# Performance work log

Hardware: AMD Instinct MI355X
Metric: run time of the kernel (lower is better)

Reference implementation:

```python
import math
import jax, jax.numpy as jnp
import numpy as np

B, N, L, E, H, T = 64, 8, 128, 768, 12, 64


def setup_inputs() -> dict:
    key = jax.random.key(0)
    ks = jax.random.split(key, 8)
    s = 0.02
    return {
        "x":  jax.random.normal(ks[0], (B, N, L, E), dtype=jnp.float32),
        # torch Linear weights are [out, in]
        "Wq": jax.random.normal(ks[1], (H, E, E), dtype=jnp.float32) * s,
        "bq": jax.random.normal(ks[2], (H, E), dtype=jnp.float32) * s,
        "Wv": jax.random.normal(ks[3], (H, T, E), dtype=jnp.float32) * s,
        "bv": jax.random.normal(ks[4], (H, T), dtype=jnp.float32) * s,
        "Wf": jax.random.normal(ks[5], (E, H * T), dtype=jnp.float32) * s,
        "bf": jax.random.normal(ks[6], (E,), dtype=jnp.float32) * s,
    }


def reference(x, Wq, bq, Wv, bv, Wf, bf):
    b, n, l, e = x.shape
    S = b * n                      # set_size after the view(-1, L, E)
    x2 = x.reshape(S, l, e)
    # per-head query projection (batched over heads)
    Q = jnp.einsum('sle,hfe->hslf', x2, Wq) + bq[:, None, None, :]      # [H,S,L,E]
    # raw (unsoftmaxed) attention: (Q K^T) V / sqrt(E)
    scores = jnp.einsum('hslf,smf->hslm', Q, x2)                        # [H,S,L,L]
    attn = jnp.einsum('hslm,sme->hsle', scores, x2) * (1.0 / math.sqrt(e))
    # per-head value projection to transformer_dim
    V = jnp.einsum('hsle,hte->hslt', attn, Wv) + bv[:, None, None, :]   # [H,S,L,T]
    # concat heads along last dim (head order preserved)
    cat = jnp.transpose(V, (1, 2, 0, 3)).reshape(S, l, -1)              # [S,L,H*T]
    out = cat @ Wf.T + bf                                               # [S,L,E]
    return out.reshape(b, n, l, e)
```

## Files before the change

### kernel.cpp

```cpp
#include <hip/hip_runtime.h>
#include <stdint.h>


#define EE 768
#define SLOT 50331648L

typedef short s16x8 __attribute__((ext_vector_type(8)));
typedef float f32x4 __attribute__((ext_vector_type(4)));

__device__ __forceinline__ short f2bf(float f){
  union { float fv; uint32_t u; } v; v.fv = f;
  uint32_t r = (v.u + 0x7fffu + ((v.u >> 16) & 1u)) >> 16;
  return (short)r;
}

__device__ __forceinline__ void gld_lds16(const short* g, short* l){
  __builtin_amdgcn_global_load_lds(
      (const __attribute__((address_space(1))) void*)(uintptr_t)g,
      (__attribute__((address_space(3))) void*)(uintptr_t)l,
      16, 0, 0);
}

__device__ __forceinline__ int xcd_swz(int bid, int nwg){
  int xcd = bid & 7, loc = bid >> 3;
  int q = nwg >> 3, r = nwg & 7;
  return (xcd < r ? xcd * (q + 1) : r * (q + 1) + (xcd - r) * q) + loc;
}

__device__ __forceinline__ int swz64(int row, int c){ return c ^ ((row & 7) << 3); }
__device__ __forceinline__ int swz32(int row, int c){ return c ^ (((row >> 1) & 3) << 3); }

__global__ __launch_bounds__(256) void cast_bf16_k(const float* __restrict__ src,
                                                   short* __restrict__ dst,
                                                   long n, float scale){
  long i = ((long)blockIdx.x * 256 + threadIdx.x) * 8;
  if(i >= n) return;
  float4 a = *(const float4*)(src + i);
  float4 b = *(const float4*)(src + i + 4);
  s16x8 o;
  o[0]=f2bf(a.x*scale); o[1]=f2bf(a.y*scale); o[2]=f2bf(a.z*scale); o[3]=f2bf(a.w*scale);
  o[4]=f2bf(b.x*scale); o[5]=f2bf(b.y*scale); o[6]=f2bf(b.z*scale); o[7]=f2bf(b.w*scale);
  *(s16x8*)(dst + i) = o;
}

__global__ __launch_bounds__(256) void cvec_k(const float* __restrict__ Wf,
                                              const float* __restrict__ bv,
                                              const float* __restrict__ bfv,
                                              float* __restrict__ c){
  int e = blockIdx.x * 256 + threadIdx.x;
  if(e >= EE) return;
  float s = bfv[e];
  for(int k = 0; k < EE; ++k) s += Wf[(long)e * EE + k] * bv[k];
  c[e] = s;
}

__global__ __launch_bounds__(256) void bias_build(const float* __restrict__ bq,
                                                  float* __restrict__ biasQP){
  int i = blockIdx.x * 256 + threadIdx.x;
  if(i < 9984) biasQP[i] = (i < 9216) ? bq[i] : 0.f;
}

__global__ __launch_bounds__(512, 1) void gemm8p(const short* __restrict__ A,
                                                 const short* __restrict__ W,
                                                 const float* __restrict__ bias,
                                                 short* __restrict__ OutBase,
                                                 int hBase, int nSub, int pSub){
  extern __shared__ short lds[];
  const int tid = threadIdx.x, lane = tid & 63, w = tid >> 6;
  const int wr = w >> 2, wc = w & 3;
  const int bid = xcd_swz(blockIdx.x, nSub * 768);
  const int g = bid / 768, rb = bid - g * 768;
  const int rowBlk = rb / 3, colBlk = rb - rowBlk * 3;
  const long rowA0 = (long)rowBlk * 256;
  const int colB0 = colBlk * 256;
  const int wh = (g == pSub) ? 12 : hBase + g;
  const short* Bm = W + (long)wh * 589824L;

  const int srow = tid >> 3;
  const int ssw = swz64(srow, (tid & 7) * 8);
  const short* gA = A + (rowA0 + srow) * 768 + ssw;
  const short* gB = Bm + (long)(colB0 + srow) * 768 + ssw;

  auto stageH = [&](int b, int kt, int which){
    const short* gs = (which < 2 ? gA : gB) + (long)(which & 1) * 98304 + kt;
    short* dst = lds + b * 32768 + (which >> 1) * 16384 + (which & 1) * 8192 + w * 512;
    gld_lds16(gs, dst);
    gld_lds16(gs + 49152, dst + 4096);
  };

  f32x4 acc[8][4] = {};
  const int fr = lane & 15, fcb = (lane >> 4) * 8;
  s16x8 af[4][2], bf[2][2];

  auto readA = [&](int b, int mh){
    const short* Al = lds + b * 32768;
    #pragma unroll
    for(int m = 0; m < 4; ++m){
      int row = wr * 128 + (mh * 4 + m) * 16 + fr;
      #pragma unroll
      for(int kk = 0; kk < 2; ++kk)
        af[m][kk] = *(const s16x8*)&Al[row * 64 + swz64(row, kk * 32 + fcb)];
    }
  };
  auto readB = [&](int b, int nh){
    const short* Bl = lds + b * 32768 + 16384;
    #pragma unroll
    for(int n = 0; n < 2; ++n){
      int row = wc * 64 + (nh * 2 + n) * 16 + fr;
      #pragma unroll
      for(int kk = 0; kk < 2; ++kk)
        bf[n][kk] = *(const s16x8*)&Bl[row * 64 + swz64(row, kk * 32 + fcb)];
    }
  };
  auto mmq = [&](int mh, int nh){
    asm volatile("s_waitcnt lgkmcnt(0)" ::: "memory");
    __builtin_amdgcn_s_setprio(1);
    #pragma unroll
    for(int m = 0; m < 4; ++m)
      #pragma unroll
      for(int n = 0; n < 2; ++n)
        #pragma unroll
        for(int kk = 0; kk < 2; ++kk)
          acc[mh*4+m][nh*2+n] = __builtin_amdgcn_mfma_f32_16x16x32_bf16(
              af[m][kk], bf[n][kk], acc[mh*4+m][nh*2+n], 0, 0, 0);
    __builtin_amdgcn_s_setprio(0);
  };

  stageH(0, 0, 0); stageH(0, 0, 1); stageH(0, 0, 2); stageH(0, 0, 3);

  for(int t = 0; t < 12; ++t){
    const int b = t & 1, nb = b ^ 1;
    const int kt1 = (t + 1) * 64;
    if(t < 11){
      stageH(nb, kt1, 0);
      asm volatile("s_waitcnt vmcnt(2)" ::: "memory");
    } else {
      asm volatile("s_waitcnt vmcnt(0)" ::: "memory");
    }
    asm volatile("s_barrier" ::: "memory");
    readA(b, 0); readB(b, 0);
    mmq(0, 0);
    asm volatile("s_barrier" ::: "memory");
    readB(b, 1);
    if(t < 11) stageH(nb, kt1, 1);
    asm volatile("s_barrier" ::: "memory");
    mmq(0, 1);
    asm volatile("s_barrier" ::: "memory");
    readA(b, 1);
    if(t < 11) stageH(nb, kt1, 2);
    asm volatile("s_barrier" ::: "memory");
    mmq(1, 1);
    asm volatile("s_barrier" ::: "memory");
    readB(b, 0);
    if(t < 11) stageH(nb, kt1, 3);
    asm volatile("s_barrier" ::: "memory");
    mmq(1, 0);
    asm volatile("s_barrier" ::: "memory");
  }

  asm volatile("s_waitcnt vmcnt(0) lgkmcnt(0)" ::: "memory");
  __syncthreads();

  float bb[4];
  #pragma unroll
  for(int n = 0; n < 4; ++n)
    bb[n] = bias[wh * 768 + colB0 + wc * 64 + n * 16 + fr];

  short* Out = OutBase + (long)g * SLOT;
  short* Cs = lds;
  #pragma unroll
  for(int ch = 0; ch < 2; ++ch){
    __syncthreads();
    if(wr == ch){
      #pragma unroll
      for(int m = 0; m < 8; ++m)
        #pragma unroll
        for(int n = 0; n < 4; ++n)
          #pragma unroll
          for(int r2 = 0; r2 < 4; ++r2){
            int row = m * 16 + (lane >> 4) * 4 + r2;
            int c = wc * 64 + n * 16 + fr;
            Cs[row * 256 + (c ^ (((row >> 2) & 3) << 4))] = f2bf(acc[m][n][r2] + bb[n]);
          }
    }
    __syncthreads();
    #pragma unroll
    for(int i = 0; i < 8; ++i){
      int idx = i * 512 + tid;
      int row = idx >> 5, cl = (idx & 31) * 8;
      s16x8 v = *(const s16x8*)&Cs[row * 256 + (cl ^ (((row >> 2) & 3) << 4))];
      *(s16x8*)&Out[(rowA0 + ch * 128 + row) * 768 + colB0 + cl] = v;
    }
  }
}

__global__ __launch_bounds__(512, 1) void gemm256(const short* __restrict__ A,
                                                  const short* __restrict__ W,
                                                  const float* __restrict__ bias,
                                                  short* __restrict__ OutBase,
                                                  int hBase, int nSub, int pSub){
  __shared__ short lds[2][16384];
  const int tid = threadIdx.x, lane = tid & 63, w = tid >> 6;
  const int wr = w >> 2, wc = w & 3;
  const int bid = xcd_swz(blockIdx.x, nSub * 768);
  const int g = bid / 768, rb = bid - g * 768;
  const int rowBlk = rb / 3, colBlk = rb - rowBlk * 3;
  const long rowA0 = (long)rowBlk * 256;
  const int colB0 = colBlk * 256;
  const int wh = (g == pSub) ? 12 : hBase + g;
  const short* Bm = W + (long)wh * 589824L;
  short* Out = OutBase + (long)g * SLOT;

  const int sr0 = w * 32 + (lane >> 2);
  const int sr1 = sr0 + 16;
  const int scol = (lane & 3) * 8;
  const int sc0 = swz32(sr0, scol);
  const int sc1 = swz32(sr1, scol);
  const short* Ar0 = A + (rowA0 + sr0) * 768;
  const short* Ar1 = A + (rowA0 + sr1) * 768;
  const short* Br0 = Bm + (long)(colB0 + sr0) * 768;
  const short* Br1 = Bm + (long)(colB0 + sr1) * 768;

  f32x4 acc[8][4] = {};
  s16x8 af[4], bf0[2], bf1[2];
  const int fr = lane & 15, fc = (lane >> 4) * 8;

  auto stage = [&](int b, int kt){
    short* Al = &lds[b][0];
    short* Bl = &lds[b][8192];
    gld_lds16(Ar0 + kt + sc0, Al + (w * 2) * 512);
    gld_lds16(Ar1 + kt + sc1, Al + (w * 2 + 1) * 512);
    gld_lds16(Br0 + kt + sc0, Bl + (w * 2) * 512);
    gld_lds16(Br1 + kt + sc1, Bl + (w * 2 + 1) * 512);
  };

  stage(0, 0);
  for(int t = 0; t < 24; ++t){
    if(t < 23){
      stage((t + 1) & 1, (t + 1) * 32);
      asm volatile("s_waitcnt vmcnt(4)\n\ts_barrier" ::: "memory");
    } else {
      asm volatile("s_waitcnt vmcnt(0)\n\ts_barrier" ::: "memory");
    }
    const short* Al = &lds[t & 1][0];
    const short* Bl = &lds[t & 1][8192];

    auto loadA = [&](int mh){
      #pragma unroll
      for(int m = 0; m < 4; ++m){
        int row = wr * 128 + (mh * 4 + m) * 16 + fr;
        af[m] = *(const s16x8*)&Al[row * 32 + swz32(row, fc)];
      }
    };
    auto loadB = [&](int nh, s16x8* bf){
      #pragma unroll
      for(int n = 0; n < 2; ++n){
        int row = wc * 64 + (nh * 2 + n) * 16 + fr;
        bf[n] = *(const s16x8*)&Bl[row * 32 + swz32(row, fc)];
      }
    };
    auto mm = [&](int mh, int nh, s16x8* bf){
      __builtin_amdgcn_s_setprio(1);
      #pragma unroll
      for(int m = 0; m < 4; ++m)
        #pragma unroll
        for(int n = 0; n < 2; ++n)
          acc[mh * 4 + m][nh * 2 + n] = __builtin_amdgcn_mfma_f32_16x16x32_bf16(
              af[m], bf[n], acc[mh * 4 + m][nh * 2 + n], 0, 0, 0);
      __builtin_amdgcn_s_setprio(0);
    };

    loadA(0); loadB(0, bf0); mm(0, 0, bf0);
    loadB(1, bf1);           mm(0, 1, bf1);
    loadA(1);                mm(1, 1, bf1);
    loadB(0, bf0);           mm(1, 0, bf0);
    asm volatile("s_barrier" ::: "memory");
  }

  float bb[4];
  #pragma unroll
  for(int n = 0; n < 4; ++n)
    bb[n] = bias[wh * 768 + colB0 + wc * 64 + n * 16 + fr];

  short* Cs = &lds[0][0];
  #pragma unroll
  for(int ch = 0; ch < 2; ++ch){
    __syncthreads();
    if(wr == ch){
      #pragma unroll
      for(int m = 0; m < 8; ++m)
        #pragma unroll
        for(int n = 0; n < 4; ++n)
          #pragma unroll
          for(int r2 = 0; r2 < 4; ++r2){
            int row = m * 16 + (lane >> 4) * 4 + r2;
            int c = wc * 64 + n * 16 + fr;
            Cs[row * 256 + (c ^ (((row >> 2) & 3) << 4))] = f2bf(acc[m][n][r2] + bb[n]);
          }
    }
    __syncthreads();
    #pragma unroll
    for(int i = 0; i < 8; ++i){
      int idx = i * 512 + tid;
      int row = idx >> 5, cl = (idx & 31) * 8;
      s16x8 v = *(const s16x8*)&Cs[row * 256 + (cl ^ (((row >> 2) & 3) << 4))];
      *(s16x8*)&Out[(rowA0 + ch * 128 + row) * 768 + colB0 + cl] = v;
    }
  }
}

__global__ __launch_bounds__(256, 2) void gemm_f32(const short* __restrict__ A,
                                                   const short* __restrict__ B,
                                                   const float* __restrict__ bias,
                                                   float* __restrict__ Cout){
  __shared__ short smem[4 * 8192];
  const int tid = threadIdx.x, lane = tid & 63, w = tid >> 6;
  const int wr = w >> 1, wc = w & 1;
  const int nCol = 6;
  const int xcd = blockIdx.x & 7, loc = blockIdx.x >> 3;
  const int width = nCol << 3;
  const int gid = loc / width, rem = loc % width;
  const int rowBlk = (xcd << 6) + (gid << 3) + (rem & 7);
  const int colBlk = rem >> 3;
  const long rowA0 = (long)rowBlk << 7;
  const long colB0 = (long)colBlk << 7;
  const int lr = lane >> 3;
  const int sA = swz64(lr, (lane & 7) * 8);

  f32x4 acc[4][4] = {};
  auto stage = [&](int b, int kt){
    short* As = smem + b * 16384;
    #pragma unroll
    for(int it = 0; it < 4; ++it){
      int r = it * 32 + w * 8;
      gld_lds16(&A[(rowA0 + r + lr) * 768 + kt + sA], &As[r * 64]);
      gld_lds16(&B[(colB0 + r + lr) * 768 + kt + sA], &As[8192 + r * 64]);
    }
  };

  stage(0, 0);
  for(int t = 0; t < 12; ++t){
    const int cur = t & 1;
    if(t < 11){
      stage(cur ^ 1, (t + 1) * 64);
      asm volatile("s_waitcnt vmcnt(8)\n\ts_barrier" ::: "memory");
    } else {
      asm volatile("s_waitcnt vmcnt(0)\n\ts_barrier" ::: "memory");
    }
    const short* As = smem + cur * 16384;
    const short* Bs = As + 8192;
    #pragma unroll
    for(int kk = 0; kk < 2; ++kk){
      s16x8 af[4], bfr[4];
      #pragma unroll
      for(int m = 0; m < 4; ++m){
        int row = wr * 64 + m * 16 + (lane & 15);
        af[m] = *(const s16x8*)&As[row * 64 + swz64(row, kk * 32 + (lane >> 4) * 8)];
      }
      #pragma unroll
      for(int n = 0; n < 4; ++n){
        int row = wc * 64 + n * 16 + (lane & 15);
        bfr[n] = *(const s16x8*)&Bs[row * 64 + swz64(row, kk * 32 + (lane >> 4) * 8)];
      }
      #pragma unroll
      for(int m = 0; m < 4; ++m)
        #pragma unroll
        for(int n = 0; n < 4; ++n)
          acc[m][n] = __builtin_amdgcn_mfma_f32_16x16x32_bf16(af[m], bfr[n], acc[m][n], 0, 0, 0);
    }
    asm volatile("s_barrier" ::: "memory");
  }

  const long crow0 = rowA0 + wr * 64;
  const long ccol0 = colB0 + wc * 64;
  #pragma unroll
  for(int n = 0; n < 4; ++n){
    const long col = ccol0 + n * 16 + (lane & 15);
    const float bbv = bias[col];
    #pragma unroll
    for(int m = 0; m < 4; ++m)
      #pragma unroll
      for(int r = 0; r < 4; ++r){
        const long row = crow0 + m * 16 + (lane >> 4) * 4 + r;
        Cout[row * 768 + col] = acc[m][n][r] + bbv;
      }
  }
}

__global__ __launch_bounds__(256, 2) void attn_k(const short* __restrict__ Q,
                                                 const short* __restrict__ P,
                                                 const short* __restrict__ X,
                                                 short* __restrict__ Cat,
                                                 int h0, int nH){
  __shared__ short smem[4 * 8192];
  const int tid = threadIdx.x, lane = tid & 63, w = tid >> 6;
  const int wr = w >> 1, wc = w & 1;
  const int nwg = nH << 9;
  const int bid = xcd_swz(blockIdx.x, nwg);
  const int s = bid / nH, hi = bid - s * nH, h = h0 + hi;
  const long row0 = (long)s * 128;
  const int lr = lane >> 3;
  const int sA = swz64(lr, (lane & 7) * 8);

  const int pm = tid >> 3, pt0 = (tid & 7) * 8;
  s16x8 pv[4];
  #pragma unroll
  for(int i = 0; i < 4; ++i)
    pv[i] = *(const s16x8*)&P[(row0 + pm + i * 32) * 768L + h * 64 + pt0];

  f32x4 acc[4][4] = {};
  const short* Qh = Q + (long)hi * SLOT;
  auto stage = [&](int b, int kt){
    short* As = smem + b * 16384;
    #pragma unroll
    for(int it = 0; it < 4; ++it){
      int r = it * 32 + w * 8;
      gld_lds16(&Qh[(row0 + r + lr) * 768L + kt + sA], &As[r * 64]);
      gld_lds16(&X[(row0 + r + lr) * 768L + kt + sA], &As[8192 + r * 64]);
    }
  };

  stage(0, 0);
  for(int t = 0; t < 12; ++t){
    const int cur = t & 1;
    if(t < 11){
      stage(cur ^ 1, (t + 1) * 64);
      asm volatile("s_waitcnt vmcnt(8)\n\ts_barrier" ::: "memory");
    } else {
      asm volatile("s_waitcnt vmcnt(0)\n\ts_barrier" ::: "memory");
    }
    const short* As = smem + cur * 16384;
    const short* Bs = As + 8192;
    #pragma unroll
    for(int kk = 0; kk < 2; ++kk){
      s16x8 af[4], bfr[4];
      #pragma unroll
      for(int m = 0; m < 4; ++m){
        int row = wr * 64 + m * 16 + (lane & 15);
        af[m] = *(const s16x8*)&As[row * 64 + swz64(row, kk * 32 + (lane >> 4) * 8)];
      }
      #pragma unroll
      for(int n = 0; n < 4; ++n){
        int row = wc * 64 + n * 16 + (lane & 15);
        bfr[n] = *(const s16x8*)&Bs[row * 64 + swz64(row, kk * 32 + (lane >> 4) * 8)];
      }
      #pragma unroll
      for(int m = 0; m < 4; ++m)
        #pragma unroll
        for(int n = 0; n < 4; ++n)
          acc[m][n] = __builtin_amdgcn_mfma_f32_16x16x32_bf16(af[m], bfr[n], acc[m][n], 0, 0, 0);
    }
    asm volatile("s_barrier" ::: "memory");
  }

  short* Pt = smem;
  short* Vt = smem + 8192;
  short* Ss = smem + 16384;

  #pragma unroll
  for(int m = 0; m < 4; ++m)
    #pragma unroll
    for(int n = 0; n < 4; ++n)
      #pragma unroll
      for(int r = 0; r < 4; ++r){
        int row = wr * 64 + m * 16 + (lane >> 4) * 4 + r;
        int c = wc * 64 + n * 16 + (lane & 15);
        Ss[row * 128 + swz64(row, c)] = f2bf(acc[m][n][r]);
      }
  #pragma unroll
  for(int i = 0; i < 4; ++i)
    #pragma unroll
    for(int j = 0; j < 8; ++j){
      int trow = pt0 + j;
      int mc = pm + i * 32;
      Pt[trow * 128 + swz64(trow, mc)] = pv[i][j];
    }
  __syncthreads();

  f32x4 accv[2][4] = {};
  #pragma unroll
  for(int kk = 0; kk < 4; ++kk){
    s16x8 a2[2], b4[4];
    #pragma unroll
    for(int m = 0; m < 2; ++m){
      int row = w * 32 + m * 16 + (lane & 15);
      a2[m] = *(const s16x8*)&Ss[row * 128 + swz64(row, kk * 32 + (lane >> 4) * 8)];
    }
    #pragma unroll
    for(int n = 0; n < 4; ++n){
      int trow = n * 16 + (lane & 15);
      b4[n] = *(const s16x8*)&Pt[trow * 128 + swz64(trow, kk * 32 + (lane >> 4) * 8)];
    }
    #pragma unroll
    for(int m = 0; m < 2; ++m)
      #pragma unroll
      for(int n = 0; n < 4; ++n)
        accv[m][n] = __builtin_amdgcn_mfma_f32_16x16x32_bf16(a2[m], b4[n], accv[m][n], 0, 0, 0);
  }

  #pragma unroll
  for(int m = 0; m < 2; ++m)
    #pragma unroll
    for(int n = 0; n < 4; ++n)
      #pragma unroll
      for(int r = 0; r < 4; ++r){
        int row = w * 32 + m * 16 + (lane >> 4) * 4 + r;
        int c = n * 16 + (lane & 15);
        Vt[row * 64 + swz64(row, c)] = f2bf(accv[m][n][r]);
      }
  __syncthreads();
  #pragma unroll
  for(int k2 = 0; k2 < 4; ++k2){
    int row = k2 * 32 + (tid >> 3);
    int cl = (tid & 7) * 8;
    s16x8 v = *(const s16x8*)&Vt[row * 64 + swz64(row, cl)];
    *(s16x8*)&Cat[(row0 + row) * 768L + h * 64 + cl] = v;
  }
}

extern "C" void kernel_launch(void* const* d_in, const int* in_sizes, int n_in,
                              void* d_out, int out_size, void* d_ws, size_t ws_size,
                              hipStream_t stream){
  const float* x  = (const float*)d_in[0];
  const float* Wq = (const float*)d_in[1];
  const float* bq = (const float*)d_in[2];
  const float* Wv = (const float*)d_in[3];
  const float* bv = (const float*)d_in[4];
  const float* Wf = (const float*)d_in[5];
  const float* bfv= (const float*)d_in[6];

  const float rsqE = 0.03608439182435161f;
  char* ws = (char*)d_ws;

  short* Xb  = (short*)(ws);
  short* Cat = (short*)(ws + 100663296L);
  short* Wb  = (short*)(ws + 201326592L);
  short* Wfb = (short*)(ws + 216662016L);
  float* bQP = (float*)(ws + 217841664L);
  float* cv  = (float*)(ws + 217881600L);
  short* QS  = (short*)(ws + 217884672L);

  const size_t QOFF = 217884672ULL;
  int G = 1;
  const int cands[5] = {12, 6, 4, 3, 2};
  for(int i = 0; i < 5; ++i)
    if(ws_size >= QOFF + (size_t)(cands[i] + 1) * 100663296ULL){ G = cands[i]; break; }
  short* Pall = QS + (long)G * SLOT;

  bool deep = hipFuncSetAttribute(reinterpret_cast<const void*>(&gemm8p),
                  hipFuncAttributeMaxDynamicSharedMemorySize, 131072) == hipSuccess;

  dim3 b256(256), b512(512);
  cast_bf16_k<<<24576, b256, 0, stream>>>(x,  Xb, 50331648L, 1.f);
  cast_bf16_k<<<3456,  b256, 0, stream>>>(Wq, Wb, 7077888L, 1.f);
  cast_bf16_k<<<288,   b256, 0, stream>>>(Wv, Wb + 7077888L, 589824L, rsqE);
  cast_bf16_k<<<288,   b256, 0, stream>>>(Wf, Wfb, 589824L, 1.f);
  bias_build<<<39, b256, 0, stream>>>(bq, bQP);
  cvec_k<<<3, b256, 0, stream>>>(Wf, bv, bfv, cv);

  const int nB = 12 / G;
  for(int b = 0; b < nB; ++b){
    const int nSub = G + (b == 0 ? 1 : 0);
    const int pSub = (b == 0) ? G : -1;
    if(deep)
      gemm8p<<<dim3(nSub * 768), b512, 131072, stream>>>(Xb, Wb, bQP, QS, b * G, nSub, pSub);
    else
      gemm256<<<dim3(nSub * 768), b512, 0, stream>>>(Xb, Wb, bQP, QS, b * G, nSub, pSub);
    attn_k<<<dim3(G * 512), b256, 0, stream>>>(QS, Pall, Xb, Cat, b * G, G);
  }
  gemm_f32<<<dim3(3072), b256, 0, stream>>>(Cat, Wfb, cv, (float*)d_out);
}
```

Baseline: 1.680 ms.

## Pipeline attention QK stage in quarters and reuse deep GEMM for final projection

The attention kernel's first GEMM loop now issues its next-tile loads in four chunks spread across four MFMA quarter-steps. Each quarter reads only half of the A and B fragments and raises wave priority during MFMA, so loads overlap compute instead of waiting on one bulk prefetch. The final output projection now runs through the templated deep-LDS gemm8p kernel, which writes fp32 directly, in place of the separate gemm_f32 kernel. The cost is more barriers per k-step, and the fp32 epilogue stores straight from registers without LDS staging, which may reduce store coalescing.

New measurement: 1.671 ms. About the same (-0.5%).

```diff
diff --git a/kernel.cpp b/kernel.cpp
--- a/kernel.cpp
+++ b/kernel.cpp
@@ -60,10 +60,11 @@
   if(i < 9984) biasQP[i] = (i < 9216) ? bq[i] : 0.f;
 }
 
+template<bool OUTF32>
 __global__ __launch_bounds__(512, 1) void gemm8p(const short* __restrict__ A,
                                                  const short* __restrict__ W,
                                                  const float* __restrict__ bias,
-                                                 short* __restrict__ OutBase,
+                                                 void* __restrict__ OutBase,
                                                  int hBase, int nSub, int pSub){
   extern __shared__ short lds[];
   const int tid = threadIdx.x, lane = tid & 63, w = tid >> 6;
@@ -166,31 +167,45 @@
   for(int n = 0; n < 4; ++n)
     bb[n] = bias[wh * 768 + colB0 + wc * 64 + n * 16 + fr];
 
-  short* Out = OutBase + (long)g * SLOT;
-  short* Cs = lds;
-  #pragma unroll
-  for(int ch = 0; ch < 2; ++ch){
-    __syncthreads();
-    if(wr == ch){
-      #pragma unroll
-      for(int m = 0; m < 8; ++m)
+  if constexpr(!OUTF32){
+    short* Out = (short*)OutBase + (long)g * SLOT;
+    short* Cs = lds;
+    #pragma unroll
+    for(int ch = 0; ch < 2; ++ch){
+      __syncthreads();
+      if(wr == ch){
         #pragma unroll
-        for(int n = 0; n < 4; ++n)
+        for(int m = 0; m < 8; ++m)
           #pragma unroll
-          for(int r2 = 0; r2 < 4; ++r2){
-            int row = m * 16 + (lane >> 4) * 4 + r2;
-            int c = wc * 64 + n * 16 + fr;
-            Cs[row * 256 + (c ^ (((row >> 2) & 3) << 4))] = f2bf(acc[m][n][r2] + bb[n]);
-          }
-    }
-    __syncthreads();
-    #pragma unroll
-    for(int i = 0; i < 8; ++i){
-      int idx = i * 512 + tid;
-      int row = idx >> 5, cl = (idx & 31) * 8;
-      s16x8 v = *(const s16x8*)&Cs[row * 256 + (cl ^ (((row >> 2) & 3) << 4))];
-      *(s16x8*)&Out[(rowA0 + ch * 128 + row) * 768 + colB0 + cl] = v;
-    }
+          for(int n = 0; n < 4; ++n)
+            #pragma unroll
+            for(int r2 = 0; r2 < 4; ++r2){
+              int row = m * 16 + (lane >> 4) * 4 + r2;
+              int c = wc * 64 + n * 16 + fr;
+              Cs[row * 256 + (c ^ (((row >> 2) & 3) << 4))] = f2bf(acc[m][n][r2] + bb[n]);
+            }
+      }
+      __syncthreads();
+      #pragma unroll
+      for(int i = 0; i < 8; ++i){
+        int idx = i * 512 + tid;
+        int row = idx >> 5, cl = (idx & 31) * 8;
+        s16x8 v = *(const s16x8*)&Cs[row * 256 + (cl ^ (((row >> 2) & 3) << 4))];
+        *(s16x8*)&Out[(rowA0 + ch * 128 + row) * 768 + colB0 + cl] = v;
+      }
+    }
+  } else {
+    float* Co = (float*)OutBase;
+    #pragma unroll
+    for(int m = 0; m < 8; ++m)
+      #pragma unroll
+      for(int n = 0; n < 4; ++n)
+        #pragma unroll
+        for(int r2 = 0; r2 < 4; ++r2){
+          const long row = rowA0 + wr * 128 + m * 16 + (lane >> 4) * 4 + r2;
+          const int col = colB0 + wc * 64 + n * 16 + fr;
+          Co[row * 768 + col] = acc[m][n][r2] + bb[n];
+        }
   }
 }
 
@@ -399,8 +414,6 @@
   const int bid = xcd_swz(blockIdx.x, nwg);
   const int s = bid / nH, hi = bid - s * nH, h = h0 + hi;
   const long row0 = (long)s * 128;
-  const int lr = lane >> 3;
-  const int sA = swz64(lr, (lane & 7) * 8);
 
   const int pm = tid >> 3, pt0 = (tid & 7) * 8;
   s16x8 pv[4];
@@ -408,50 +421,90 @@
   for(int i = 0; i < 4; ++i)
     pv[i] = *(const s16x8*)&P[(row0 + pm + i * 32) * 768L + h * 64 + pt0];
 
+  const short* Qh = Q + (long)hi * SLOT;
+  const int srow = tid >> 3;
+  const int ssw = swz64(srow, (tid & 7) * 8);
+  const short* gQ = Qh + (row0 + srow) * 768 + ssw;
+  const short* gX = X + (row0 + srow) * 768 + ssw;
+
+  auto stageQX = [&](int b, int kt, int j){
+    short* As = smem + b * 16384;
+    gld_lds16(gQ + (long)j * 24576 + kt, As + j * 2048 + w * 512);
+    gld_lds16(gX + (long)j * 24576 + kt, As + 8192 + j * 2048 + w * 512);
+  };
+
   f32x4 acc[4][4] = {};
-  const short* Qh = Q + (long)hi * SLOT;
-  auto stage = [&](int b, int kt){
-    short* As = smem + b * 16384;
-    #pragma unroll
-    for(int it = 0; it < 4; ++it){
-      int r = it * 32 + w * 8;
-      gld_lds16(&Qh[(row0 + r + lr) * 768L + kt + sA], &As[r * 64]);
-      gld_lds16(&X[(row0 + r + lr) * 768L + kt + sA], &As[8192 + r * 64]);
-    }
-  };
-
-  stage(0, 0);
+  const int fr = lane & 15, fcb = (lane >> 4) * 8;
+  s16x8 af[2][2], bf[2][2];
+
+  auto readAq = [&](int b, int mh){
+    const short* Al = smem + b * 16384;
+    #pragma unroll
+    for(int m = 0; m < 2; ++m){
+      int row = wr * 64 + (mh * 2 + m) * 16 + fr;
+      #pragma unroll
+      for(int kk = 0; kk < 2; ++kk)
+        af[m][kk] = *(const s16x8*)&Al[row * 64 + swz64(row, kk * 32 + fcb)];
+    }
+  };
+  auto readBq = [&](int b, int nh){
+    const short* Bl = smem + b * 16384 + 8192;
+    #pragma unroll
+    for(int n = 0; n < 2; ++n){
+      int row = wc * 64 + (nh * 2 + n) * 16 + fr;
+      #pragma unroll
+      for(int kk = 0; kk < 2; ++kk)
+        bf[n][kk] = *(const s16x8*)&Bl[row * 64 + swz64(row, kk * 32 + fcb)];
+    }
+  };
+  auto mmq = [&](int mh, int nh){
+    asm volatile("s_waitcnt lgkmcnt(0)" ::: "memory");
+    __builtin_amdgcn_s_setprio(1);
+    #pragma unroll
+    for(int m = 0; m < 2; ++m)
+      #pragma unroll
+      for(int n = 0; n < 2; ++n)
+        #pragma unroll
+        for(int kk = 0; kk < 2; ++kk)
+          acc[mh*2+m][nh*2+n] = __builtin_amdgcn_mfma_f32_16x16x32_bf16(
+              af[m][kk], bf[n][kk], acc[mh*2+m][nh*2+n], 0, 0, 0);
+    __builtin_amdgcn_s_setprio(0);
+  };
+
+  stageQX(0, 0, 0); stageQX(0, 0, 1); stageQX(0, 0, 2); stageQX(0, 0, 3);
+
   for(int t = 0; t < 12; ++t){
-    const int cur = t & 1;
+    const int b = t & 1, nb = b ^ 1;
+    const int kt1 = (t + 1) * 64;
     if(t < 11){
-      stage(cur ^ 1, (t + 1) * 64);
-      asm volatile("s_waitcnt vmcnt(8)\n\ts_barrier" ::: "memory");
+      stageQX(nb, kt1, 0);
+      asm volatile("s_waitcnt vmcnt(2)" ::: "memory");
     } else {
-      asm volatile("s_waitcnt vmcnt(0)\n\ts_barrier" ::: "memory");
-    }
-    const short* As = smem + cur * 16384;
-    const short* Bs = As + 8192;
-    #pragma unroll
-    for(int kk = 0; kk < 2; ++kk){
-      s16x8 af[4], bfr[4];
-      #pragma unroll
-      for(int m = 0; m < 4; ++m){
-        int row = wr * 64 + m * 16 + (lane & 15);
-        af[m] = *(const s16x8*)&As[row * 64 + swz64(row, kk * 32 + (lane >> 4) * 8)];
-      }
-      #pragma unroll
-      for(int n = 0; n < 4; ++n){
-        int row = wc * 64 + n * 16 + (lane & 15);
-        bfr[n] = *(const s16x8*)&Bs[row * 64 + swz64(row, kk * 32 + (lane >> 4) * 8)];
-      }
-      #pragma unroll
-      for(int m = 0; m < 4; ++m)
-        #pragma unroll
-        for(int n = 0; n < 4; ++n)
-          acc[m][n] = __builtin_amdgcn_mfma_f32_16x16x32_bf16(af[m], bfr[n], acc[m][n], 0, 0, 0);
-    }
-    asm volatile("s_barrier" ::: "memory");
-  }
+      asm volatile("s_waitcnt vmcnt(0)" ::: "memory");
+    }
+    asm volatile("s_barrier" ::: "memory");
+    readAq(b, 0); readBq(b, 0);
+    mmq(0, 0);
+    asm volatile("s_barrier" ::: "memory");
+    readBq(b, 1);
+    if(t < 11) stageQX(nb, kt1, 1);
+    asm volatile("s_barrier" ::: "memory");
+    mmq(0, 1);
+    asm volatile("s_barrier" ::: "memory");
+    readAq(b, 1);
+    if(t < 11) stageQX(nb, kt1, 2);
+    asm volatile("s_barrier" ::: "memory");
+    mmq(1, 1);
+    asm volatile("s_barrier" ::: "memory");
+    readBq(b, 0);
+    if(t < 11) stageQX(nb, kt1, 3);
+    asm volatile("s_barrier" ::: "memory");
+    mmq(1, 0);
+    asm volatile("s_barrier" ::: "memory");
+  }
+
+  asm volatile("s_waitcnt vmcnt(0) lgkmcnt(0)" ::: "memory");
+  __syncthreads();
 
   short* Pt = smem;
   short* Vt = smem + 8192;
@@ -547,8 +600,11 @@
     if(ws_size >= QOFF + (size_t)(cands[i] + 1) * 100663296ULL){ G = cands[i]; break; }
   short* Pall = QS + (long)G * SLOT;
 
-  bool deep = hipFuncSetAttribute(reinterpret_cast<const void*>(&gemm8p),
-                  hipFuncAttributeMaxDynamicSharedMemorySize, 131072) == hipSuccess;
+  bool deep =
+      hipFuncSetAttribute(reinterpret_cast<const void*>(&gemm8p<false>),
+                          hipFuncAttributeMaxDynamicSharedMemorySize, 131072) == hipSuccess &&
+      hipFuncSetAttribute(reinterpret_cast<const void*>(&gemm8p<true>),
+                          hipFuncAttributeMaxDynamicSharedMemorySize, 131072) == hipSuccess;
 
   dim3 b256(256), b512(512);
   cast_bf16_k<<<24576, b256, 0, stream>>>(x,  Xb, 50331648L, 1.f);
@@ -563,10 +619,13 @@
     const int nSub = G + (b == 0 ? 1 : 0);
     const int pSub = (b == 0) ? G : -1;
     if(deep)
-      gemm8p<<<dim3(nSub * 768), b512, 131072, stream>>>(Xb, Wb, bQP, QS, b * G, nSub, pSub);
+      gemm8p<false><<<dim3(nSub * 768), b512, 131072, stream>>>(Xb, Wb, bQP, QS, b * G, nSub, pSub);
     else
       gemm256<<<dim3(nSub * 768), b512, 0, stream>>>(Xb, Wb, bQP, QS, b * G, nSub, pSub);
     attn_k<<<dim3(G * 512), b256, 0, stream>>>(QS, Pall, Xb, Cat, b * G, G);
   }
-  gemm_f32<<<dim3(3072), b256, 0, stream>>>(Cat, Wfb, cv, (float*)d_out);
-}
+  if(deep)
+    gemm8p<true><<<dim3(768), b512, 131072, stream>>>(Cat, Wfb, cv, d_out, 0, 1, -1);
+  else
+    gemm_f32<<<dim3(3072), b256, 0, stream>>>(Cat, Wfb, cv, (float*)d_out);
+}
```
